# Performance work log

Hardware: AMD Instinct MI355X
Metric: run time of the kernel (lower is better)

## Reference

```python
import jax, jax.numpy as jnp
import numpy as np

B, D_IN, D, C = 64, 1024, 768, 1000
EPS = 0.1        # args.alpha_cap
NUM_SIM = 3      # args.num_sim


def setup_inputs() -> dict:
    key = jax.random.key(0)
    k0, k1, k2, k3 = jax.random.split(key, 4)
    return {
        "x": jax.random.normal(k0, (B, D_IN), jnp.float32),
        "W_emb": jax.random.normal(k1, (D, D_IN), jnp.float32) * 0.02,
        "b_emb": jnp.zeros((D,), jnp.float32),
        "W_fc": jax.random.normal(k2, (C, D), jnp.float32) * 0.02,
        "b_fc": jnp.zeros((C,), jnp.float32),
        "anchors": jax.random.normal(k3, (C, D), jnp.float32),
    }


def _forward_core(x, W_emb, b_emb, W_fc, b_fc, anchors):
    # self.embedding(x): feature extractor -> [B, D]
    emb = x @ W_emb.T + b_emb
    # self.model(x) head logits -> [B, C]
    logits = emb @ W_fc.T + b_fc
    # compute_ulb_grads: grad of CE(fc(emb), onehot_j) wrt emb = (softmax - onehot_j) @ W_fc.
    # softmax is shared across all pseudo-labels j, so grad_ij = G_i - W_fc[j].
    p = jax.nn.softmax(logits, axis=-1)          # [B, C]
    G = p @ W_fc                                  # [B, D]
    grads = G[:, None, :] - W_fc[None, :, :]      # [B, C, D]
    # calculate_optimum_alpha: z = anchor - ulb_embed
    z = anchors[None, :, :] - emb[:, None, :]     # [B, C, D]
    z_norm = jnp.linalg.norm(z, axis=-1, keepdims=True)        # [B, C, 1]
    g_norm = jnp.linalg.norm(grads, axis=-1, keepdims=True)    # [B, C, 1]
    alpha = (EPS * z_norm / g_norm) * grads / (z + 1e-8)       # [B, C, D]
    # mix_feature: (1-alpha)*ulb_embed + alpha*anchor
    mix = (1.0 - alpha) * emb[:, None, :] + alpha * anchors[None, :, :]  # [B, C, D]
    # fc(feature_mix) -> [B, C, C]
    logits_mix = jnp.einsum('bjd,cd->bjc', mix, W_fc) + b_fc
    return logits, logits_mix


def reference(x, W_emb, b_emb, W_fc, b_fc, anchors):
    logits, logits_mix = _forward_core(x, W_emb, b_emb, W_fc, b_fc, anchors)
    predictions = jnp.argmax(logits, axis=-1)       # [B]
    preds_mix = jnp.argmax(logits_mix, axis=-1)     # [B, C]
    counts = jnp.zeros((B, C), jnp.float32)
    counts = counts.at[jnp.arange(B), predictions].add(1.0)
    counts = counts.at[jnp.arange(B)[:, None], preds_mix].add(1.0)
    # all_below_threshold: labels_count < num_sample everywhere
    return jnp.all(counts < NUM_SIM, axis=1)
```

## Files before the change

### kernel.cpp

```cpp
#include <hip/hip_runtime.h>
#include <stdint.h>
#include <stddef.h>

#define BB 64
#define DIN 1024
#define DD 768
#define CC 1000
#define EPSA 0.1f
#define NSIM 3

typedef short  s16x8 __attribute__((ext_vector_type(8)));
typedef float  f32x4 __attribute__((ext_vector_type(4)));

static __device__ __forceinline__ unsigned short f2bf_rne(float x) {
  unsigned u = __float_as_uint(x);
  return (unsigned short)((u + 0x7FFFu + ((u >> 16) & 1u)) >> 16);
}
static __device__ __forceinline__ float bf2f(unsigned short h) {
  return __uint_as_float(((unsigned)h) << 16);
}

__global__ __launch_bounds__(256) void prep_kernel(const float* __restrict__ W_fc,
                                                   const float* __restrict__ anchors,
                                                   const float* __restrict__ W_emb,
                                                   const float* __restrict__ x,
                                                   short* __restrict__ Bp, short* __restrict__ Ap,
                                                   short* __restrict__ Ip, short* __restrict__ Xp,
                                                   float* __restrict__ An2) {
  const int blk = blockIdx.x, tid = threadIdx.x;
  if (blk < 1184) {
    const float* src; short* dst; int KS, nrow, gid;
    if (blk < 384)       { src = W_fc;    dst = Bp; KS = 24; nrow = CC;  gid = blk * 256 + tid; }
    else if (blk < 768)  { src = anchors; dst = Ap; KS = 24; nrow = CC;  gid = (blk - 384) * 256 + tid; }
    else if (blk < 1152) { src = W_emb;   dst = Ip; KS = 32; nrow = DD;  gid = (blk - 768) * 256 + tid; }
    else                 { src = x;       dst = Xp; KS = 32; nrow = BB;  gid = (blk - 1152) * 256 + tid; }
    int lane = gid & 63;
    int ks   = (gid >> 6) % KS;
    int nt   = gid / (64 * KS);
    int row  = nt * 16 + (lane & 15);
    int k0   = ks * 32 + (lane >> 4) * 8;
    int stride = KS * 32;
    s16x8 v;
    #pragma unroll
    for (int r = 0; r < 8; ++r) {
      float w = (row < nrow) ? src[(size_t)row * stride + k0 + r] : 0.0f;
      v[r] = (short)f2bf_rne(w);
    }
    ((s16x8*)dst)[gid] = v;
  } else {
    int w = tid >> 6, lane = tid & 63;
    int j = (blk - 1184) * 4 + w;
    const float4* ar = (const float4*)(anchors + (size_t)j * DD);
    float an = 0.f;
    for (int k4 = lane; k4 < DD / 4; k4 += 64) {
      float4 a = ar[k4];
      an += a.x*a.x + a.y*a.y + a.z*a.z + a.w*a.w;
    }
    #pragma unroll
    for (int o = 1; o < 64; o <<= 1) an += __shfl_xor(an, o);
    if (lane == 0) An2[j] = an;
  }
}

__global__ __launch_bounds__(256) void embV_kernel(const short* __restrict__ Bp,
                                                   const short* __restrict__ Ip,
                                                   const short* __restrict__ Xp,
                                                   const float* __restrict__ b_emb,
                                                   unsigned short* __restrict__ Vb,
                                                   float* __restrict__ emb) {
  const int tid = threadIdx.x, w = tid >> 6, lane = tid & 63;
  if (blockIdx.x < 256) {
    const int bx = blockIdx.x & 15, cb = blockIdx.x >> 4;
    const int rnt = bx * 4 + w;
    const s16x8* BH = (const s16x8*)Bp;
    f32x4 acc[4] = {};
    for (int ks = 0; ks < 24; ++ks) {
      s16x8 a = BH[(rnt * 24 + ks) * 64 + lane];
      #pragma unroll
      for (int nf = 0; nf < 4; ++nf)
        acc[nf] = __builtin_amdgcn_mfma_f32_16x16x32_bf16(a, BH[((cb * 4 + nf) * 24 + ks) * 64 + lane], acc[nf], 0, 0, 0);
    }
    const int r0 = rnt * 16 + (lane >> 4) * 4;
    const int c0 = cb * 64 + (lane & 15);
    #pragma unroll
    for (int nf = 0; nf < 4; ++nf)
      #pragma unroll
      for (int rr = 0; rr < 4; ++rr)
        Vb[(size_t)(r0 + rr) * 1024 + c0 + nf * 16] = f2bf_rne(acc[nf][rr]);
  } else {
    const int g = blockIdx.x - 256;
    const int nfr = g * 4 + w;
    const s16x8* XH = (const s16x8*)Xp;
    const s16x8* IH = (const s16x8*)Ip;
    f32x4 acc[4] = {};
    for (int ks = 0; ks < 32; ++ks) {
      s16x8 b = IH[(nfr * 32 + ks) * 64 + lane];
      #pragma unroll
      for (int mt = 0; mt < 4; ++mt)
        acc[mt] = __builtin_amdgcn_mfma_f32_16x16x32_bf16(XH[(mt * 32 + ks) * 64 + lane], b, acc[mt], 0, 0, 0);
    }
    const int d = nfr * 16 + (lane & 15);
    const float be = b_emb[d];
    #pragma unroll
    for (int mt = 0; mt < 4; ++mt)
      #pragma unroll
      for (int rr = 0; rr < 4; ++rr)
        emb[(size_t)(mt * 16 + (lane >> 4) * 4 + rr) * DD + d] = acc[mt][rr] + be;
  }
}

__global__ __launch_bounds__(256) void packmid_kernel(const unsigned short* __restrict__ Vb,
                                                      const float* __restrict__ emb,
                                                      short* __restrict__ Vp,
                                                      short* __restrict__ Ep) {
  const int blk = blockIdx.x, tid = threadIdx.x;
  if (blk < 512) {
    int gid = blk * 256 + tid;
    int lane = gid & 63, ks = (gid >> 6) % 32, nt = gid / (64 * 32);
    int row = nt * 16 + (lane & 15);
    int k0  = ks * 32 + (lane >> 4) * 8;
    ((s16x8*)Vp)[gid] = *(const s16x8*)(Vb + (size_t)row * 1024 + k0);
  } else {
    int gid = (blk - 512) * 256 + tid;
    if (gid >= 4 * 24 * 64) return;
    int lane = gid & 63, ks = (gid >> 6) % 24, mt = gid / (64 * 24);
    int row = mt * 16 + (lane & 15);
    int k0  = ks * 32 + (lane >> 4) * 8;
    s16x8 v;
    #pragma unroll
    for (int r = 0; r < 8; ++r) v[r] = (short)f2bf_rne(emb[(size_t)row * DD + k0 + r]);
    ((s16x8*)Ep)[gid] = v;
  }
}

__global__ __launch_bounds__(64) void logitsAE_kernel(const short* __restrict__ Ep,
                                                      const short* __restrict__ Bp,
                                                      const short* __restrict__ Ap,
                                                      const float* __restrict__ b_fc,
                                                      float* __restrict__ logits,
                                                      float* __restrict__ AE) {
  const int nfr = blockIdx.x;
  const int mt  = blockIdx.y;
  const int lane = threadIdx.x;
  const s16x8* E = (const s16x8*)Ep;
  const s16x8* B = (const s16x8*)Bp;
  const s16x8* A = (const s16x8*)Ap;
  f32x4 accL = {}, accA = {};
  for (int ks = 0; ks < 24; ++ks) {
    s16x8 a  = E[(mt * 24 + ks) * 64 + lane];
    s16x8 bW = B[(nfr * 24 + ks) * 64 + lane];
    s16x8 bA = A[(nfr * 24 + ks) * 64 + lane];
    accL = __builtin_amdgcn_mfma_f32_16x16x32_bf16(a, bW, accL, 0, 0, 0);
    accA = __builtin_amdgcn_mfma_f32_16x16x32_bf16(a, bA, accA, 0, 0, 0);
  }
  const int c = nfr * 16 + (lane & 15);
  if (c < CC) {
    const float bf = b_fc[c];
    #pragma unroll
    for (int rr = 0; rr < 4; ++rr) {
      int b = mt * 16 + (lane >> 4) * 4 + rr;
      logits[b * CC + c] = accL[rr] + bf;
      AE[b * CC + c]     = accA[rr];
    }
  }
}

__global__ __launch_bounds__(256) void softmax_kernel(const float* __restrict__ logits,
                                                      const float* __restrict__ emb,
                                                      float* __restrict__ p,
                                                      short* __restrict__ Pp,
                                                      int* __restrict__ pred,
                                                      float* __restrict__ En2) {
  int b = blockIdx.x, t = threadIdx.x;
  __shared__ float smax[256];
  __shared__ int   sidx[256];
  __shared__ float ssum[256];
  {
    float pe = 0.f;
    for (int k = t; k < DD; k += 256) { float e = emb[b * DD + k]; pe += e * e; }
    #pragma unroll
    for (int o = 1; o < 64; o <<= 1) pe += __shfl_xor(pe, o);
    __shared__ float se[4];
    if ((t & 63) == 0) se[t >> 6] = pe;
    __syncthreads();
    if (t == 0) En2[b] = se[0] + se[1] + se[2] + se[3];
  }
  float m = -3.402823466e38f; int mi = 0;
  for (int c = t; c < CC; c += 256) {
    float v = logits[b * CC + c];
    if (v > m) { m = v; mi = c; }
  }
  smax[t] = m; sidx[t] = mi;
  __syncthreads();
  for (int o = 128; o > 0; o >>= 1) {
    if (t < o) {
      float v2 = smax[t + o]; int i2 = sidx[t + o];
      if (v2 > smax[t] || (v2 == smax[t] && i2 < sidx[t])) { smax[t] = v2; sidx[t] = i2; }
    }
    __syncthreads();
  }
  float M = smax[0];
  if (t == 0) pred[b] = sidx[0];
  float sum = 0.f;
  for (int c = t; c < CC; c += 256) sum += expf(logits[b * CC + c] - M);
  ssum[t] = sum;
  __syncthreads();
  for (int o = 128; o > 0; o >>= 1) {
    if (t < o) ssum[t] += ssum[t + o];
    __syncthreads();
  }
  float S = ssum[0];
  const int mt = b >> 4, blo = b & 15;
  for (int j = t; j < CC; j += 256) {
    float pj = expf(logits[b * CC + j] - M) / S;
    p[b * CC + j] = pj;
    size_t fi = ((size_t)(mt * 32 + (j >> 5)) * 64 + ((j >> 3) & 3) * 16 + blo) * 8 + (j & 7);
    Pp[fi] = (short)f2bf_rne(pj);
  }
  if (t < 24) {
    int j = 1000 + t;
    size_t fi = ((size_t)(mt * 32 + (j >> 5)) * 64 + ((j >> 3) & 3) * 16 + blo) * 8 + (j & 7);
    Pp[fi] = 0;
  }
}

__global__ __launch_bounds__(64) void u_kernel(const short* __restrict__ Pp,
                                               const short* __restrict__ Vp,
                                               float* __restrict__ u) {
  const int nfr = blockIdx.x;
  const int mt  = blockIdx.y;
  const int lane = threadIdx.x;
  const s16x8* P = (const s16x8*)Pp;
  const s16x8* V = (const s16x8*)Vp;
  f32x4 acc = {};
  for (int ks = 0; ks < 32; ++ks) {
    s16x8 b = V[(nfr * 32 + ks) * 64 + lane];
    acc = __builtin_amdgcn_mfma_f32_16x16x32_bf16(P[(mt * 32 + ks) * 64 + lane], b, acc, 0, 0, 0);
  }
  const int c = nfr * 16 + (lane & 15);
  if (c < CC) {
    #pragma unroll
    for (int rr = 0; rr < 4; ++rr)
      u[(mt * 16 + (lane >> 4) * 4 + rr) * CC + c] = acc[rr];
  }
}

__global__ __launch_bounds__(256) void scan_kernel(const float* __restrict__ logits,
                                                   const float* __restrict__ u,
                                                   const float* __restrict__ p,
                                                   const float* __restrict__ AE,
                                                   const float* __restrict__ An2,
                                                   const float* __restrict__ En2,
                                                   const unsigned short* __restrict__ Vb,
                                                   unsigned long long* __restrict__ part) {
  const int b = blockIdx.x, cz = blockIdx.y;
  const int tid = threadIdx.x;
  const int c0 = cz * 125;
  __shared__ __attribute__((aligned(8))) float2 LU[128];
  __shared__ float se[4];

  if (tid < 125) {
    int c = c0 + tid;
    LU[tid] = float2{logits[b * CC + c], u[b * CC + c]};
  }
  float partsum = 0.f;
  {
    int cg = tid * 4;
    if (cg + 3 < CC) {
      float4 p4 = *(const float4*)(p + b * CC + cg);
      float4 u4 = *(const float4*)(u + b * CC + cg);
      partsum = p4.x*u4.x + p4.y*u4.y + p4.z*u4.z + p4.w*u4.w;
    } else {
      #pragma unroll
      for (int i = 0; i < 4; ++i) {
        int c = cg + i;
        if (c < CC) partsum += p[b * CC + c] * u[b * CC + c];
      }
    }
  }
  #pragma unroll
  for (int o = 1; o < 64; o <<= 1) partsum += __shfl_xor(partsum, o);
  if ((tid & 63) == 0) se[tid >> 6] = partsum;
  __syncthreads();
  const float gn2b = se[0] + se[1] + se[2] + se[3];
  const float en2 = En2[b];

  const int jt = (tid < 250 ? tid : 249) * 4;
  float4 an4 = *(const float4*)(An2 + jt);
  float4 ae4 = *(const float4*)(AE + b * CC + jt);
  float4 uj4 = *(const float4*)(u + b * CC + jt);
  float sj[4], nsj[4];
  {
    float anv[4] = {an4.x, an4.y, an4.z, an4.w};
    float aev[4] = {ae4.x, ae4.y, ae4.z, ae4.w};
    float ujv[4] = {uj4.x, uj4.y, uj4.z, uj4.w};
    #pragma unroll
    for (int k = 0; k < 4; ++k) {
      float vd  = bf2f(Vb[(size_t)(jt + k) * 1024 + jt + k]);
      float zn2 = anv[k] - 2.0f * aev[k] + en2;
      float gn2 = gn2b - 2.0f * ujv[k] + vd;
      sj[k] = (EPSA * sqrtf(zn2)) / sqrtf(gn2);
      nsj[k] = -sj[k];
    }
  }

  float best[4] = {-3.402823466e38f, -3.402823466e38f, -3.402823466e38f, -3.402823466e38f};
  int   bi[4]   = {0, 0, 0, 0};
  const unsigned short* Vcol = Vb + jt;
  #pragma unroll 5
  for (int i = 0; i < 125; ++i) {
    int c = c0 + i;
    float2 lu = LU[i];
    uint2 vv = *(const uint2*)(Vcol + (size_t)c * 1024);
    float v0 = __uint_as_float(vv.x << 16);
    float v1 = __uint_as_float(vv.x & 0xffff0000u);
    float v2 = __uint_as_float(vv.y << 16);
    float v3 = __uint_as_float(vv.y & 0xffff0000u);
    float t0 = fmaf(sj[0], lu.y, lu.x);
    float t1 = fmaf(sj[1], lu.y, lu.x);
    float t2 = fmaf(sj[2], lu.y, lu.x);
    float t3 = fmaf(sj[3], lu.y, lu.x);
    float val0 = fmaf(nsj[0], v0, t0);
    float val1 = fmaf(nsj[1], v1, t1);
    float val2 = fmaf(nsj[2], v2, t2);
    float val3 = fmaf(nsj[3], v3, t3);
    if (val0 > best[0]) { best[0] = val0; bi[0] = c; }
    if (val1 > best[1]) { best[1] = val1; bi[1] = c; }
    if (val2 > best[2]) { best[2] = val2; bi[2] = c; }
    if (val3 > best[3]) { best[3] = val3; bi[3] = c; }
  }

  if (tid < 250) {
    unsigned long long* dst = part + (size_t)cz * 64000 + b * 1000 + jt;
    #pragma unroll
    for (int k = 0; k < 4; ++k) {
      unsigned ub = __float_as_uint(best[k]);
      ub = (ub & 0x80000000u) ? ~ub : (ub | 0x80000000u);
      dst[k] = ((unsigned long long)ub << 32) |
               (unsigned long long)(0xFFFFFFFFu - (unsigned)bi[k]);
    }
  }
}

__global__ __launch_bounds__(256) void counts_kernel(const unsigned long long* __restrict__ part,
                                                     const int* __restrict__ pred,
                                                     float* __restrict__ out) {
  int b = blockIdx.x, t = threadIdx.x;
  __shared__ int cnt[CC];
  __shared__ int bad;
  for (int c = t; c < CC; c += 256) cnt[c] = 0;
  if (t == 0) bad = 0;
  __syncthreads();
  if (t == 0) atomicAdd(&cnt[pred[b]], 1);
  const unsigned long long* pr = part + b * 1000;
  for (int j = t; j < CC; j += 256) {
    unsigned long long key = 0;
    #pragma unroll
    for (int cz = 0; cz < 8; ++cz) {
      unsigned long long k2 = pr[(size_t)cz * 64000 + j];
      key = (k2 > key) ? k2 : key;
    }
    int c = (int)(0xFFFFFFFFu - (unsigned)(key & 0xFFFFFFFFull));
    atomicAdd(&cnt[c], 1);
  }
  __syncthreads();
  for (int c = t; c < CC; c += 256) if (cnt[c] >= NSIM) bad = 1;
  __syncthreads();
  if (t == 0) out[b] = bad ? 0.0f : 1.0f;
}

extern "C" void kernel_launch(void* const* d_in, const int* in_sizes, int n_in,
                              void* d_out, int out_size, void* d_ws, size_t ws_size,
                              hipStream_t stream) {
  const float* x       = (const float*)d_in[0];
  const float* W_emb   = (const float*)d_in[1];
  const float* b_emb   = (const float*)d_in[2];
  const float* W_fc    = (const float*)d_in[3];
  const float* b_fc    = (const float*)d_in[4];
  const float* anchors = (const float*)d_in[5];
  float* out = (float*)d_out;

  float* emb    = (float*)d_ws;
  float* logits = emb + BB * DD;
  float* p      = logits + BB * CC;
  float* u      = p + BB * CC;
  float* AE     = u + BB * CC;
  float* An2    = AE + BB * CC;
  float* En2    = An2 + 1024;
  int*   pred   = (int*)(En2 + 64);
  unsigned long long* part = (unsigned long long*)(pred + 64);
  short* Bp     = (short*)(part + 8 * 64000);
  short* Ap     = Bp + 64 * 24 * 64 * 8;
  short* Ip     = Ap + 64 * 24 * 64 * 8;
  short* Xp     = Ip + 48 * 32 * 64 * 8;
  short* Ep     = Xp + 4 * 32 * 64 * 8;
  short* Pp     = Ep + 4 * 24 * 64 * 8;
  unsigned short* Vb = (unsigned short*)(Pp + 4 * 32 * 64 * 8);
  short* Vp     = (short*)(Vb + 1024 * 1024);

  hipLaunchKernelGGL(prep_kernel,    dim3(1434), dim3(256), 0, stream,
                     W_fc, anchors, W_emb, x, Bp, Ap, Ip, Xp, An2);
  hipLaunchKernelGGL(embV_kernel,    dim3(268), dim3(256), 0, stream, Bp, Ip, Xp, b_emb, Vb, emb);
  hipLaunchKernelGGL(packmid_kernel, dim3(536), dim3(256), 0, stream, Vb, emb, Vp, Ep);
  hipLaunchKernelGGL(logitsAE_kernel,dim3(64, 4), dim3(64), 0, stream, Ep, Bp, Ap, b_fc, logits, AE);
  hipLaunchKernelGGL(softmax_kernel, dim3(BB), dim3(256), 0, stream, logits, emb, p, Pp, pred, En2);
  hipLaunchKernelGGL(u_kernel,       dim3(64, 4), dim3(64), 0, stream, Pp, Vp, u);
  hipLaunchKernelGGL(scan_kernel,    dim3(BB, 8), dim3(256), 0, stream,
                     logits, u, p, AE, An2, En2, Vb, part);
  hipLaunchKernelGGL(counts_kernel,  dim3(BB), dim3(256), 0, stream, part, pred, out);
}
```

Before: 73.19 us.

## Fuse operand packing into embV epilogue and split scan over more chunks

The separate packmid kernel is removed. embV now stages its bf16 outputs in shared memory and writes the MFMA-packed Vp and Ep layouts directly from its epilogue, which saves one launch and a full re-read of Vb and emb. The scan kernel also splits the class dimension into 16 chunks of 63 instead of 8 chunks of 125, giving twice the blocks for more parallelism. The cost is twice the partial-result buffer traffic in counts, plus a block-wide barrier in embV.

```diff
diff --git a/kernel.cpp b/kernel.cpp
--- a/kernel.cpp
+++ b/kernel.cpp
@@ -67,8 +67,11 @@
                                                    const short* __restrict__ Xp,
                                                    const float* __restrict__ b_emb,
                                                    unsigned short* __restrict__ Vb,
-                                                   float* __restrict__ emb) {
+                                                   short* __restrict__ Vp,
+                                                   float* __restrict__ emb,
+                                                   short* __restrict__ Ep) {
   const int tid = threadIdx.x, w = tid >> 6, lane = tid & 63;
+  __shared__ __attribute__((aligned(16))) short lsh[4608];
   if (blockIdx.x < 256) {
     const int bx = blockIdx.x & 15, cb = blockIdx.x >> 4;
     const int rnt = bx * 4 + w;
@@ -80,13 +83,24 @@
       for (int nf = 0; nf < 4; ++nf)
         acc[nf] = __builtin_amdgcn_mfma_f32_16x16x32_bf16(a, BH[((cb * 4 + nf) * 24 + ks) * 64 + lane], acc[nf], 0, 0, 0);
     }
-    const int r0 = rnt * 16 + (lane >> 4) * 4;
+    const int rl0 = (lane >> 4) * 4;
+    const int r0 = rnt * 16 + rl0;
     const int c0 = cb * 64 + (lane & 15);
     #pragma unroll
     for (int nf = 0; nf < 4; ++nf)
       #pragma unroll
-      for (int rr = 0; rr < 4; ++rr)
-        Vb[(size_t)(r0 + rr) * 1024 + c0 + nf * 16] = f2bf_rne(acc[nf][rr]);
+      for (int rr = 0; rr < 4; ++rr) {
+        unsigned short h = f2bf_rne(acc[nf][rr]);
+        Vb[(size_t)(r0 + rr) * 1024 + c0 + nf * 16] = h;
+        lsh[w * 1152 + (rl0 + rr) * 72 + (lane & 15) + nf * 16] = (short)h;
+      }
+    __syncthreads();
+    #pragma unroll
+    for (int ksh = 0; ksh < 2; ++ksh) {
+      int ks = cb * 2 + ksh;
+      s16x8 v = *(const s16x8*)&lsh[w * 1152 + (lane & 15) * 72 + ksh * 32 + (lane >> 4) * 8];
+      ((s16x8*)Vp)[(rnt * 32 + ks) * 64 + lane] = v;
+    }
   } else {
     const int g = blockIdx.x - 256;
     const int nfr = g * 4 + w;
@@ -100,36 +114,25 @@
         acc[mt] = __builtin_amdgcn_mfma_f32_16x16x32_bf16(XH[(mt * 32 + ks) * 64 + lane], b, acc[mt], 0, 0, 0);
     }
     const int d = nfr * 16 + (lane & 15);
+    const int dl = w * 16 + (lane & 15);
     const float be = b_emb[d];
     #pragma unroll
     for (int mt = 0; mt < 4; ++mt)
       #pragma unroll
-      for (int rr = 0; rr < 4; ++rr)
-        emb[(size_t)(mt * 16 + (lane >> 4) * 4 + rr) * DD + d] = acc[mt][rr] + be;
-  }
-}
-
-__global__ __launch_bounds__(256) void packmid_kernel(const unsigned short* __restrict__ Vb,
-                                                      const float* __restrict__ emb,
-                                                      short* __restrict__ Vp,
-                                                      short* __restrict__ Ep) {
-  const int blk = blockIdx.x, tid = threadIdx.x;
-  if (blk < 512) {
-    int gid = blk * 256 + tid;
-    int lane = gid & 63, ks = (gid >> 6) % 32, nt = gid / (64 * 32);
-    int row = nt * 16 + (lane & 15);
-    int k0  = ks * 32 + (lane >> 4) * 8;
-    ((s16x8*)Vp)[gid] = *(const s16x8*)(Vb + (size_t)row * 1024 + k0);
-  } else {
-    int gid = (blk - 512) * 256 + tid;
-    if (gid >= 4 * 24 * 64) return;
-    int lane = gid & 63, ks = (gid >> 6) % 24, mt = gid / (64 * 24);
-    int row = mt * 16 + (lane & 15);
-    int k0  = ks * 32 + (lane >> 4) * 8;
-    s16x8 v;
-    #pragma unroll
-    for (int r = 0; r < 8; ++r) v[r] = (short)f2bf_rne(emb[(size_t)row * DD + k0 + r]);
-    ((s16x8*)Ep)[gid] = v;
+      for (int rr = 0; rr < 4; ++rr) {
+        int b = mt * 16 + (lane >> 4) * 4 + rr;
+        float ev = acc[mt][rr] + be;
+        emb[(size_t)b * DD + d] = ev;
+        lsh[b * 72 + dl] = (short)f2bf_rne(ev);
+      }
+    __syncthreads();
+    #pragma unroll
+    for (int ksh = 0; ksh < 2; ++ksh) {
+      int ks = g * 2 + ksh;
+      int mt2 = tid >> 6;
+      s16x8 v = *(const s16x8*)&lsh[(mt2 * 16 + (lane & 15)) * 72 + ksh * 32 + (lane >> 4) * 8];
+      ((s16x8*)Ep)[(mt2 * 24 + ks) * 64 + lane] = v;
+    }
   }
 }
 
@@ -255,11 +258,12 @@
                                                    unsigned long long* __restrict__ part) {
   const int b = blockIdx.x, cz = blockIdx.y;
   const int tid = threadIdx.x;
-  const int c0 = cz * 125;
-  __shared__ __attribute__((aligned(8))) float2 LU[128];
+  const int c0 = cz * 63;
+  const int cend = (CC - c0 < 63) ? (CC - c0) : 63;
+  __shared__ __attribute__((aligned(8))) float2 LU[64];
   __shared__ float se[4];
 
-  if (tid < 125) {
+  if (tid < cend) {
     int c = c0 + tid;
     LU[tid] = float2{logits[b * CC + c], u[b * CC + c]};
   }
@@ -307,8 +311,8 @@
   float best[4] = {-3.402823466e38f, -3.402823466e38f, -3.402823466e38f, -3.402823466e38f};
   int   bi[4]   = {0, 0, 0, 0};
   const unsigned short* Vcol = Vb + jt;
-  #pragma unroll 5
-  for (int i = 0; i < 125; ++i) {
+  #pragma unroll 7
+  for (int i = 0; i < cend; ++i) {
     int c = c0 + i;
     float2 lu = LU[i];
     uint2 vv = *(const uint2*)(Vcol + (size_t)c * 1024);
@@ -356,7 +360,7 @@
   for (int j = t; j < CC; j += 256) {
     unsigned long long key = 0;
     #pragma unroll
-    for (int cz = 0; cz < 8; ++cz) {
+    for (int cz = 0; cz < 16; ++cz) {
       unsigned long long k2 = pr[(size_t)cz * 64000 + j];
       key = (k2 > key) ? k2 : key;
     }
@@ -389,7 +393,7 @@
   float* En2    = An2 + 1024;
   int*   pred   = (int*)(En2 + 64);
   unsigned long long* part = (unsigned long long*)(pred + 64);
-  short* Bp     = (short*)(part + 8 * 64000);
+  short* Bp     = (short*)(part + 16 * 64000);
   short* Ap     = Bp + 64 * 24 * 64 * 8;
   short* Ip     = Ap + 64 * 24 * 64 * 8;
   short* Xp     = Ip + 48 * 32 * 64 * 8;
@@ -400,12 +404,12 @@
 
   hipLaunchKernelGGL(prep_kernel,    dim3(1434), dim3(256), 0, stream,
                      W_fc, anchors, W_emb, x, Bp, Ap, Ip, Xp, An2);
-  hipLaunchKernelGGL(embV_kernel,    dim3(268), dim3(256), 0, stream, Bp, Ip, Xp, b_emb, Vb, emb);
-  hipLaunchKernelGGL(packmid_kernel, dim3(536), dim3(256), 0, stream, Vb, emb, Vp, Ep);
+  hipLaunchKernelGGL(embV_kernel,    dim3(268), dim3(256), 0, stream,
+                     Bp, Ip, Xp, b_emb, Vb, Vp, emb, Ep);
   hipLaunchKernelGGL(logitsAE_kernel,dim3(64, 4), dim3(64), 0, stream, Ep, Bp, Ap, b_fc, logits, AE);
   hipLaunchKernelGGL(softmax_kernel, dim3(BB), dim3(256), 0, stream, logits, emb, p, Pp, pred, En2);
   hipLaunchKernelGGL(u_kernel,       dim3(64, 4), dim3(64), 0, stream, Pp, Vp, u);
-  hipLaunchKernelGGL(scan_kernel,    dim3(BB, 8), dim3(256), 0, stream,
+  hipLaunchKernelGGL(scan_kernel,    dim3(BB, 16), dim3(256), 0, stream,
                      logits, u, p, AE, An2, En2, Vb, part);
   hipLaunchKernelGGL(counts_kernel,  dim3(BB), dim3(256), 0, stream, part, pred, out);
 }
```

New measurement: 73.37 us. Within noise of the previous version (+0.2%).
